# Optimization experiments

Measured on AMD Instinct MI355X. Metric: run time of the kernel, lower is better.

Reference implementation:

```python
import jax, jax.numpy as jnp
import numpy as np

B, S = 16, 128
V_W, V_C = 32000, 128
E, CD, H, L, CLS = 300, 50, 100, 20, 3
EPS = 1e-8


def _lstm(x, Wih, Whh, b):
    # x: (B, T, I); PyTorch gate order i, f, g, o
    Bb, Hh = x.shape[0], Whh.shape[1]
    def step(carry, xt):
        h, c = carry
        z = xt @ Wih.T + h @ Whh.T + b
        i, f, g, o = jnp.split(z, 4, axis=-1)
        c = jax.nn.sigmoid(f) * c + jax.nn.sigmoid(i) * jnp.tanh(g)
        h = jax.nn.sigmoid(o) * jnp.tanh(c)
        return (h, c), h
    h0 = jnp.zeros((Bb, Hh), x.dtype)
    (hT, _), hs = jax.lax.scan(step, (h0, h0), x.swapaxes(0, 1))
    return hs.swapaxes(0, 1), hT  # (B,T,H), (B,H)


def _bilstm_out(x, Wf, Uf, bf, Wb, Ub, bb):
    of, _ = _lstm(x, Wf, Uf, bf)
    ob, _ = _lstm(x[:, ::-1], Wb, Ub, bb)
    return of, ob[:, ::-1]


def _agg_last(x, Wf, Uf, bf, Wb, Ub, bb):
    _, hf = _lstm(x, Wf, Uf, bf)
    _, hb = _lstm(x[:, ::-1], Wb, Ub, bb)
    return jnp.concatenate([hf, hb], -1)  # (B, 2H)


def _mp_match(v1, v2, w):
    # cos(w_l * v1, w_l * v2) without materializing (B,S,H,L)
    if v2.ndim == 2:
        v2 = v2[:, None, :]
    ws = w * w  # (L,H)
    num = jnp.einsum('bsh,lh->bsl', v1 * v2, ws)
    n1 = jnp.sqrt(jnp.einsum('bsh,lh->bsl', v1 * v1, ws))
    n2 = jnp.sqrt(jnp.einsum('bsh,lh->bsl', v2 * v2, ws))
    return num / jnp.maximum(n1 * n2, EPS)


def _cos_att(v1, v2):
    a = jnp.einsum('bph,bqh->bpq', v1, v2)
    n1 = jnp.linalg.norm(v1, axis=2)[:, :, None]
    n2 = jnp.linalg.norm(v2, axis=2)[:, None, :]
    return a / jnp.maximum(n1 * n2, EPS)


def _branch(p_fw, p_bw, h_fw, h_bw, w1, w2, w3, w4, w5, w6):
    mp_full_fw = _mp_match(p_fw, h_fw[:, -1, :], w1)
    mp_full_bw = _mp_match(p_bw, h_bw[:, 0, :], w2)
    mh_full_fw = _mp_match(h_fw, p_fw[:, -1, :], w1)
    mh_full_bw = _mp_match(h_bw, p_bw[:, 0, :], w2)

    def att_feats(pv, hv):
        att = _cos_att(pv, hv)  # (B,P,Q)
        mean_h = jnp.einsum('bpq,bqh->bph', att, hv) / jnp.maximum(att.sum(2, keepdims=True), EPS)
        mean_p = jnp.einsum('bpq,bph->bqh', att, pv) / jnp.maximum(att.sum(1)[:, :, None], EPS)
        max_h = jnp.max(hv[:, None, :, :] * att[..., None], axis=2)  # (B,P,H)
        max_p = jnp.max(pv[:, :, None, :] * att[..., None], axis=1)  # (B,Q,H)
        return mean_h, mean_p, max_h, max_p

    mean_h_fw, mean_p_fw, max_h_fw, max_p_fw = att_feats(p_fw, h_fw)
    mean_h_bw, mean_p_bw, max_h_bw, max_p_bw = att_feats(p_bw, h_bw)

    mp_mean_fw = _mp_match(p_fw, mean_h_fw, w3)
    mp_mean_bw = _mp_match(p_bw, mean_h_bw, w4)
    mh_mean_fw = _mp_match(h_fw, mean_p_fw, w3)
    mh_mean_bw = _mp_match(h_bw, mean_p_bw, w4)
    mp_max_fw = _mp_match(p_fw, max_h_fw, w5)
    mp_max_bw = _mp_match(p_bw, max_h_bw, w6)
    mh_max_fw = _mp_match(h_fw, max_p_fw, w5)
    mh_max_bw = _mp_match(h_bw, max_p_bw, w6)

    mv_p = jnp.concatenate([mp_full_fw, mp_mean_fw, mp_max_fw, mp_full_bw, mp_mean_bw, mp_max_bw], 2)
    mv_h = jnp.concatenate([mh_full_fw, mh_mean_fw, mh_max_fw, mh_full_bw, mh_mean_bw, mh_max_bw], 2)
    return mv_p, mv_h  # (B,S,6L)


def _highway(x, lw, lb, gw, gb):
    hlin = jax.nn.relu(x @ lw.T + lb)
    t = jax.nn.sigmoid(x @ gw.T + gb)
    return t * hlin + (1.0 - t) * x


def setup_inputs():
    key = jax.random.key(0)
    keys = iter(jax.random.split(key, 80))
    def rn(*shape):
        return jax.random.normal(next(keys), shape, jnp.float32) * 0.1
    d = {}
    d['p_ids'] = jax.random.randint(next(keys), (B, S), 0, V_W)
    d['h_ids'] = jax.random.randint(next(keys), (B, S), 0, V_W)
    d['cp_ids'] = jax.random.randint(next(keys), (B, S), 0, V_C)
    d['ch_ids'] = jax.random.randint(next(keys), (B, S), 0, V_C)
    d['word_emb'] = rn(V_W, E)
    d['char_emb'] = rn(V_C, CD)
    for pref, inp in (('ctx', E), ('chr', CD), ('agg', 6 * L)):
        for dd in ('f', 'b'):
            d[pref + '_Wih_' + dd] = rn(4 * H, inp)
            d[pref + '_Whh_' + dd] = rn(4 * H, H)
            d[pref + '_b_' + dd] = jnp.zeros((4 * H,), jnp.float32)
    for i in range(1, 7):
        d['mp_w%d' % i] = rn(L, H)
    d['char_w1'] = rn(L, H)
    d['char_w2'] = rn(L, H)
    d['hw_lin_w'] = rn(4 * H, 4 * H)
    d['hw_lin_b'] = jnp.zeros((4 * H,), jnp.float32)
    d['hw_gate_w'] = rn(4 * H, 4 * H)
    d['hw_gate_b'] = jnp.zeros((4 * H,), jnp.float32)
    d['fc1_w'] = rn(2 * H, 8 * H)
    d['fc1_b'] = jnp.zeros((2 * H,), jnp.float32)
    d['fc2_w'] = rn(CLS, 2 * H)
    d['fc2_b'] = jnp.zeros((CLS,), jnp.float32)
    return d


def reference(p_ids, h_ids, cp_ids, ch_ids, word_emb, char_emb,
              ctx_Wih_f, ctx_Whh_f, ctx_b_f, ctx_Wih_b, ctx_Whh_b, ctx_b_b,
              chr_Wih_f, chr_Whh_f, chr_b_f, chr_Wih_b, chr_Whh_b, chr_b_b,
              agg_Wih_f, agg_Whh_f, agg_b_f, agg_Wih_b, agg_Whh_b, agg_b_b,
              mp_w1, mp_w2, mp_w3, mp_w4, mp_w5, mp_w6, char_w1, char_w2,
              hw_lin_w, hw_lin_b, hw_gate_w, hw_gate_b, fc1_w, fc1_b, fc2_w, fc2_b):
    agg = (agg_Wih_f, agg_Whh_f, agg_b_f, agg_Wih_b, agg_Whh_b, agg_b_b)
    ctx = (ctx_Wih_f, ctx_Whh_f, ctx_b_f, ctx_Wih_b, ctx_Whh_b, ctx_b_b)
    chr_ = (chr_Wih_f, chr_Whh_f, chr_b_f, chr_Wih_b, chr_Whh_b, chr_b_b)

    # word path
    p_fw, p_bw = _bilstm_out(word_emb[p_ids], *ctx)
    h_fw, h_bw = _bilstm_out(word_emb[h_ids], *ctx)
    mv_p, mv_h = _branch(p_fw, p_bw, h_fw, h_bw, mp_w1, mp_w2, mp_w3, mp_w4, mp_w5, mp_w6)
    wx = jnp.concatenate([_agg_last(mv_p, *agg), _agg_last(mv_h, *agg)], -1)  # (B,4H)

    # char path (code applies mp_w3..6 to char branch; requires char_hidden == hidden)
    cp_fw, cp_bw = _bilstm_out(char_emb[cp_ids], *chr_)
    ch_fw, ch_bw = _bilstm_out(char_emb[ch_ids], *chr_)
    cmv_p, cmv_h = _branch(cp_fw, cp_bw, ch_fw, ch_bw, char_w1, char_w2, mp_w3, mp_w4, mp_w5, mp_w6)
    cx = jnp.concatenate([_agg_last(cmv_p, *agg), _agg_last(cmv_h, *agg)], -1)  # (B,4H)

    wx = _highway(wx, hw_lin_w, hw_lin_b, hw_gate_w, hw_gate_b)
    cx = _highway(cx, hw_lin_w, hw_lin_b, hw_gate_w, hw_gate_b)
    x = jnp.tanh(jnp.concatenate([wx, cx], -1) @ fc1_w.T + fc1_b)
    return x @ fc2_w.T + fc2_b  # (B, CLS)
```

## Files before the change

### kernel.cpp

```cpp
#include <hip/hip_runtime.h>


#define Bz 16
#define Sz 128
#define Hz 100
#define Gz 400
#define NT 25
#define EPSV 1e-8f

#define XIN_CH  ((long)Sz * Bz * Gz)
#define HOUT_CH ((long)Bz * Sz * Hz)
#define MV_CH   ((long)Bz * Sz * 120)

typedef __attribute__((ext_vector_type(4))) float floatx4;
typedef __attribute__((ext_vector_type(8))) __bf16 bf16x8;

union FragU { bf16x8 v; unsigned u[4]; unsigned short s[8]; };

__device__ __forceinline__ float bf2f(unsigned short h) {
  unsigned u = ((unsigned)h) << 16;
  return __builtin_bit_cast(float, u);
}
__device__ __forceinline__ unsigned short f2bf(float x) {
  unsigned u = __builtin_bit_cast(unsigned, x);
  u = u + 0x7FFFu + ((u >> 16) & 1u);
  return (unsigned short)(u >> 16);
}
__device__ __forceinline__ float rcpf(float x) { return __builtin_amdgcn_rcpf(x); }
__device__ __forceinline__ float sigf(float x) { return rcpf(1.0f + __expf(-x)); }
__device__ __forceinline__ float tanh_fast(float x) {
  return 1.0f - 2.0f * rcpf(__expf(2.0f * x) + 1.0f);
}

__device__ __forceinline__ void barrier_lds_only() {
  __asm__ __volatile__("s_waitcnt lgkmcnt(0)\ns_barrier" ::: "memory");
}

#define MFMA(a, b, c) __builtin_amdgcn_mfma_f32_16x16x32_bf16((a), (b), (c), 0, 0, 0)

__device__ __forceinline__ int pv_chain(int grp) { return (grp < 2 ? 0 : 4) + (grp & 1); }

struct CvtDesc { const float* src; unsigned short* dst; int K; int KP; };
struct Cvt6 { CvtDesc d[6]; };

__global__ __launch_bounds__(64) void k_cvt(Cvt6 C) {
  int bx = blockIdx.x;
  int m = bx / Gz;
  int p = bx % Gz;
  CvtDesc d = C.d[m];
  int orig = (p & 3) * Hz + (p >> 2);
  const float* src = d.src + (long)orig * d.K;
  unsigned short* dst = d.dst + (long)p * d.KP;
  for (int k = threadIdx.x; k < d.KP; k += 64)
    dst[k] = (k < d.K) ? f2bf(src[k]) : 0;
}

struct ProjChain {
  const int* ids;
  const float* emb;
  const float* src;
  const unsigned short* W16;
  const float* bias;
  float* out;
  int rev;
  int K;
  int nch;
};
struct Proj8 { ProjChain c[8]; };

#define PPS 328

__global__ __launch_bounds__(256) void k_proj(Proj8 P) {
  __shared__ __align__(16) unsigned short phi[16 * PPS];
  __shared__ __align__(16) unsigned short plo[16 * PPS];

  int bx = blockIdx.x;
  int c = bx >> 7;
  int t = bx & 127;
  const ProjChain ch = P.c[c];
  const int K = ch.K;
  const int KP = ch.nch * 32;
  int tp = ch.rev ? (Sz - 1 - t) : t;
  int tid = threadIdx.x;

  for (int i = tid; i < 16 * KP; i += 256) {
    int b = i / KP, k = i % KP;
    float v = 0.f;
    if (k < K) {
      const float* row = ch.ids ? (ch.emb + (long)ch.ids[b * Sz + tp] * K)
                                : (ch.src + ((long)b * Sz + tp) * K);
      v = row[k];
    }
    unsigned u = __builtin_bit_cast(unsigned, v);
    phi[b * PPS + k] = (unsigned short)(u >> 16);
    float hi = __builtin_bit_cast(float, u & 0xFFFF0000u);
    unsigned ul = __builtin_bit_cast(unsigned, v - hi);
    plo[b * PPS + k] = (unsigned short)(ul >> 16);
  }
  __syncthreads();

  int w = tid >> 6, lane = tid & 63;
  int nl = lane & 15, qd = lane >> 4;
  floatx4 acc[7];
#pragma unroll
  for (int i = 0; i < 7; ++i) acc[i] = floatx4{0.f, 0.f, 0.f, 0.f};

  const unsigned short* wbase[7];
#pragma unroll
  for (int i = 0; i < 7; ++i) {
    int nt = w + 4 * i;
    wbase[i] = (nt < NT) ? (ch.W16 + (long)(nt * 16 + nl) * KP) : ch.W16;
  }

  for (int cc = 0; cc < ch.nch; ++cc) {
    FragU bhi, blo;
    bhi.v = *(const bf16x8*)&phi[nl * PPS + cc * 32 + qd * 8];
    blo.v = *(const bf16x8*)&plo[nl * PPS + cc * 32 + qd * 8];
    int ko = cc * 32 + qd * 8;
#pragma unroll
    for (int i = 0; i < 7; ++i) {
      if (w + 4 * i < NT) {
        FragU whi;
        whi.v = *(const bf16x8*)(wbase[i] + ko);
        acc[i] = MFMA(whi.v, bhi.v, acc[i]);
        acc[i] = MFMA(whi.v, blo.v, acc[i]);
      }
    }
  }
#pragma unroll
  for (int i = 0; i < 7; ++i) {
    int nt = w + 4 * i;
    if (nt < NT) {
#pragma unroll
      for (int r = 0; r < 4; ++r) {
        int p = nt * 16 + qd * 4 + r;
        acc[i][r] += ch.bias[(p & 3) * Hz + (p >> 2)];
      }
      *(floatx4*)(ch.out + ((long)t * Bz + nl) * Gz + nt * 16 + qd * 4) = acc[i];
    }
  }
}

struct LstmChain {
  const float* xin;
  const float* Whh;
  float* hout;
  int rev;
  int store_all;
};
struct Lstm8 { LstmChain c[8]; };

#define NW 16
#define TPW 2
#define NCH 4
#define HPR 160

__global__ __launch_bounds__(1024, 4) void k_lstm(Lstm8 P) {
  __shared__ __align__(16) unsigned short hhi[2][Bz * HPR];
  __shared__ __align__(16) unsigned short hlo[2][Bz * HPR];
  __shared__ float hfp[2][Bz * Hz];

  const LstmChain ch = P.c[blockIdx.x];
  const int tid = threadIdx.x;
  const int w = tid >> 6;
  const int lane = tid & 63;
  const int nl = lane & 15;
  const int qd = lane >> 4;

  for (int i = tid; i < Bz * HPR; i += 1024) {
    ((unsigned*)hhi)[i] = 0;
    ((unsigned*)hlo)[i] = 0;
  }
  __syncthreads();

  FragU wa[TPW][NCH];
#pragma unroll
  for (int i = 0; i < TPW; ++i) {
    int tile = i * NW + w;
    if (tile < NT) {
      int pA = tile * 16 + nl;
      const float* wr = ch.Whh + (long)((pA & 3) * Hz + (pA >> 2)) * Hz;
#pragma unroll
      for (int cc = 0; cc < NCH; ++cc) {
#pragma unroll
        for (int j = 0; j < 8; ++j) {
          int k = cc * 32 + qd * 8 + j;
          wa[i][cc].s[j] = f2bf((k < Hz) ? wr[k] : 0.f);
        }
      }
    }
  }

  long hbase[2]; int hok[2]; int hidx[2];
#pragma unroll
  for (int it = 0; it < 2; ++it) {
    int idx = tid + it * 1024;
    hok[it] = idx < Bz * Hz;
    int bq = idx / Hz, rq = idx - bq * Hz;
    hbase[it] = (long)bq * Sz * Hz + rq;
    hidx[it] = idx;
  }

  floatx4 xc[TPW], xn[TPW];
  float cstate[TPW];
#pragma unroll
  for (int i = 0; i < TPW; ++i) {
    cstate[i] = 0.f;
    xc[i] = floatx4{0.f, 0.f, 0.f, 0.f};
    if (i * NW + w < NT)
      xc[i] = *(const floatx4*)(ch.xin + (long)nl * Gz + (i * NW + w) * 16 + qd * 4);
  }

  for (int t = 0; t < Sz; ++t) {
    if (ch.store_all && t > 0) {
      int pb = (t - 1) & 1;
      int sprev = ch.rev ? (Sz - t) : (t - 1);
#pragma unroll
      for (int it = 0; it < 2; ++it)
        if (hok[it])
          ch.hout[hbase[it] + (long)sprev * Hz] = hfp[pb][hidx[it]];
    }
    if (t + 1 < Sz) {
      const float* xp = ch.xin + (long)(t + 1) * Bz * Gz + (long)nl * Gz;
#pragma unroll
      for (int i = 0; i < TPW; ++i)
        if (i * NW + w < NT)
          xn[i] = *(const floatx4*)(xp + (i * NW + w) * 16 + qd * 4);
    }
    const int rp = t & 1;
    floatx4 acc[TPW];
#pragma unroll
    for (int i = 0; i < TPW; ++i) acc[i] = xc[i];
#pragma unroll
    for (int cc = 0; cc < NCH; ++cc) {
      FragU bhi, blo;
      bhi.v = *(const bf16x8*)(&hhi[rp][nl * HPR + cc * 32 + qd * 8]);
      blo.v = *(const bf16x8*)(&hlo[rp][nl * HPR + cc * 32 + qd * 8]);
#pragma unroll
      for (int i = 0; i < TPW; ++i)
        if (i * NW + w < NT) {
          acc[i] = MFMA(wa[i][cc].v, bhi.v, acc[i]);
          acc[i] = MFMA(wa[i][cc].v, blo.v, acc[i]);
        }
    }
    const int wp = rp ^ 1;
    const bool keep = ch.store_all || (t == Sz - 1);
#pragma unroll
    for (int i = 0; i < TPW; ++i) {
      int tile = i * NW + w;
      if (tile < NT) {
        float cn = sigf(acc[i][1]) * cstate[i] + sigf(acc[i][0]) * tanh_fast(acc[i][2]);
        float h = sigf(acc[i][3]) * tanh_fast(cn);
        cstate[i] = cn;
        int hd = tile * 4 + qd;
        unsigned u = __builtin_bit_cast(unsigned, h);
        float hi = __builtin_bit_cast(float, u & 0xFFFF0000u);
        unsigned ul = __builtin_bit_cast(unsigned, h - hi);
        hhi[wp][nl * HPR + hd] = (unsigned short)(u >> 16);
        hlo[wp][nl * HPR + hd] = (unsigned short)(ul >> 16);
        if (keep) hfp[t & 1][nl * Hz + hd] = h;
      }
    }
    barrier_lds_only();
#pragma unroll
    for (int i = 0; i < TPW; ++i) xc[i] = xn[i];
  }
  {
    int pb = (Sz - 1) & 1;
    int slast = ch.rev ? 0 : (Sz - 1);
#pragma unroll
    for (int it = 0; it < 2; ++it)
      if (hok[it])
        ch.hout[hbase[it] + (long)slast * Hz] = hfp[pb][hidx[it]];
  }
}

#define PVS2 102
#define FS 104

struct BranchArgs {
  const float* houtA;
  float* mv;
  const float* w_full[4];
  const float* w3; const float* w4; const float* w5; const float* w6;
};

__global__ __launch_bounds__(512, 1) void k_branch(BranchArgs G) {
  __shared__ float pvs[128 * PVS2];
  __shared__ float hvs[128 * PVS2 + 32];
  __shared__ float wl[60 * PVS2];
  __shared__ float attw[8 * 128];
  __shared__ float fmean[8 * FS];
  __shared__ float fmax[8 * FS];
  __shared__ float nrmp[128], nrmh[128];

  int bx = blockIdx.x;
  int grp = bx >> 6;
  int b = (bx >> 2) & 15;
  int side = (bx >> 1) & 1;
  int rh = bx & 1;
  int fw = !(grp & 1);
  int word = grp < 2;
  int pc = pv_chain(grp);
  const float* PV = G.houtA + (long)pc * HOUT_CH + (long)b * Sz * Hz;
  const float* HV = G.houtA + (long)(pc + 2) * HOUT_CH + (long)b * Sz * Hz;
  int tid = threadIdx.x;
  int w = tid >> 6, lane = tid & 63;

  for (int i = tid; i < 128 * Hz; i += 512) {
    int r = i / Hz, c = i % Hz;
    pvs[r * PVS2 + c] = PV[r * Hz + c];
    hvs[r * PVS2 + c] = HV[r * Hz + c];
  }
  {
    const float* wm = fw ? G.w3 : G.w4;
    const float* wx = fw ? G.w5 : G.w6;
    const float* wf = G.w_full[grp];
    for (int i = tid; i < 60 * Hz; i += 512) {
      int row = i / Hz, c = i % Hz;
      const float* src = (row < 20) ? wf : (row < 40 ? wm : wx);
      int rr = (row < 20) ? row : (row < 40 ? row - 20 : row - 40);
      wl[row * PVS2 + c] = src[rr * Hz + c];
    }
  }
  __syncthreads();
  if (tid < 256) {
    const float* base = (tid < 128) ? pvs : hvs;
    int r = tid & 127;
    float s = 0.f;
    for (int j = 0; j < Hz; ++j) { float v = base[r * PVS2 + j]; s += v * v; }
    if (tid < 128) nrmp[r] = sqrtf(s); else nrmh[r] = sqrtf(s);
  }
  __syncthreads();

  const float* A  = side ? hvs : pvs;
  const float* B  = side ? pvs : hvs;
  const float* nA = side ? nrmh : nrmp;
  const float* nB = side ? nrmp : nrmh;
  int bcrow = fw ? (Sz - 1) : 0;
  float* mvout = G.mv + (long)((word ? 0 : 2) + side) * MV_CH + (long)b * Sz * 120;
  int off = fw ? 0 : 60;
  int type = lane / 20;
  const float* wrow = wl + lane * PVS2;
  float* myatt = attw + w * 128;
  float* myfm = fmean + w * FS;
  float* myfx = fmax + w * FS;

  for (int task = w; task < 64; task += 8) {
    int r = rh * 64 + task;
    const float* ar = A + r * PVS2;
    float d0 = 0.f, d1 = 0.f;
    const float* b0 = B + lane * PVS2;
    const float* b1 = B + (lane + 64) * PVS2;
    for (int j = 0; j < Hz; j += 2) {
      float2 a2 = *(const float2*)(ar + j);
      float2 p2 = *(const float2*)(b0 + j);
      float2 q2 = *(const float2*)(b1 + j);
      d0 += a2.x * p2.x + a2.y * p2.y;
      d1 += a2.x * q2.x + a2.y * q2.y;
    }
    float at0 = d0 * rcpf(fmaxf(nA[r] * nB[lane], EPSV));
    float at1 = d1 * rcpf(fmaxf(nA[r] * nB[lane + 64], EPSV));
    myatt[lane] = at0;
    myatt[lane + 64] = at1;
    float s = at0 + at1;
#pragma unroll
    for (int m = 1; m < 64; m <<= 1) s += __shfl_xor(s, m);
    float inv = rcpf(fmaxf(s, EPSV));
    float m0 = 0.f, m1 = 0.f, x0 = -1e30f, x1 = -1e30f;
    const float* bj0 = B + lane;
    const float* bj1 = B + lane + 64;
    for (int q = 0; q < 128; ++q) {
      float aq = myatt[q];
      float v0 = bj0[q * PVS2];
      float v1 = bj1[q * PVS2];
      m0 += aq * v0; x0 = fmaxf(x0, aq * v0);
      m1 += aq * v1; x1 = fmaxf(x1, aq * v1);
    }
    myfm[lane] = m0 * inv;
    myfx[lane] = x0;
    if (lane < Hz - 64) { myfm[lane + 64] = m1 * inv; myfx[lane + 64] = x1; }
    if (lane < 60) {
      const float* v2p = (type == 0) ? (B + bcrow * PVS2)
                       : (type == 1) ? myfm : myfx;
      float num = 0.f, n1 = 0.f, n2 = 0.f;
      for (int j = 0; j < Hz; j += 2) {
        float2 w2 = *(const float2*)(wrow + j);
        float2 a2 = *(const float2*)(ar + j);
        float2 c2 = *(const float2*)(v2p + j);
        float ws0 = w2.x * w2.x, ws1 = w2.y * w2.y;
        num += ws0 * a2.x * c2.x + ws1 * a2.y * c2.y;
        n1  += ws0 * a2.x * a2.x + ws1 * a2.y * a2.y;
        n2  += ws0 * c2.x * c2.x + ws1 * c2.y * c2.y;
      }
      mvout[r * 120 + off + lane] = num * rcpf(fmaxf(sqrtf(n1) * sqrtf(n2), EPSV));
    }
  }
}

__global__ __launch_bounds__(1024) void k_head(const float* houtB,
                                               const float* lw, const float* lb,
                                               const float* gw, const float* gb,
                                               const float* f1w, const float* f1b,
                                               const float* f2w, const float* f2b,
                                               float* out) {
  int b = blockIdx.x;
  __shared__ float xr[800];
  __shared__ float hwv[800];
  __shared__ float f1[200];
  int tid = threadIdx.x;
  if (tid < 800) {
    int seq = tid / Gz;
    int i = tid % Gz;
    int seg = i / Hz, j = i % Hz;
    int chain = seq * 4 + seg;
    int s_sel = (seg & 1) ? 0 : (Sz - 1);
    xr[tid] = houtB[((long)chain * Bz + b) * Sz * Hz + (long)s_sel * Hz + j];
  }
  __syncthreads();
  if (tid < 800) {
    int seq = tid / Gz;
    int o = tid % Gz;
    const float* xs = xr + seq * Gz;
    const float* lwr = lw + (long)o * Gz;
    const float* gwr = gw + (long)o * Gz;
    float al = 0.f, ag = 0.f;
#pragma unroll 4
    for (int k = 0; k < Gz; ++k) {
      float x = xs[k];
      al += x * lwr[k];
      ag += x * gwr[k];
    }
    al += lb[o];
    ag += gb[o];
    float hlin = fmaxf(al, 0.f);
    float tg = sigf(ag);
    hwv[tid] = tg * hlin + (1.f - tg) * xs[o];
  }
  __syncthreads();
  if (tid < 200) {
    const float* wr = f1w + (long)tid * 800;
    float acc = f1b[tid];
#pragma unroll 4
    for (int k = 0; k < 800; ++k) acc += hwv[k] * wr[k];
    f1[tid] = tanh_fast(acc);
  }
  __syncthreads();
  if (tid < 3) {
    const float* wr = f2w + tid * 200;
    float acc = f2b[tid];
    for (int k = 0; k < 200; ++k) acc += f1[k] * wr[k];
    out[b * 3 + tid] = acc;
  }
}

extern "C" void kernel_launch(void* const* d_in, const int* in_sizes, int n_in,
                              void* d_out, int out_size, void* d_ws, size_t ws_size,
                              hipStream_t stream) {
  (void)in_sizes; (void)n_in; (void)out_size;

  const int* p_ids  = (const int*)d_in[0];
  const int* h_ids  = (const int*)d_in[1];
  const int* cp_ids = (const int*)d_in[2];
  const int* ch_ids = (const int*)d_in[3];
  const float* word_emb = (const float*)d_in[4];
  const float* char_emb = (const float*)d_in[5];
  const float* ctx_Wih_f = (const float*)d_in[6];
  const float* ctx_Whh_f = (const float*)d_in[7];
  const float* ctx_b_f   = (const float*)d_in[8];
  const float* ctx_Wih_b = (const float*)d_in[9];
  const float* ctx_Whh_b = (const float*)d_in[10];
  const float* ctx_b_b   = (const float*)d_in[11];
  const float* chr_Wih_f = (const float*)d_in[12];
  const float* chr_Whh_f = (const float*)d_in[13];
  const float* chr_b_f   = (const float*)d_in[14];
  const float* chr_Wih_b = (const float*)d_in[15];
  const float* chr_Whh_b = (const float*)d_in[16];
  const float* chr_b_b   = (const float*)d_in[17];
  const float* agg_Wih_f = (const float*)d_in[18];
  const float* agg_Whh_f = (const float*)d_in[19];
  const float* agg_b_f   = (const float*)d_in[20];
  const float* agg_Wih_b = (const float*)d_in[21];
  const float* agg_Whh_b = (const float*)d_in[22];
  const float* agg_b_b   = (const float*)d_in[23];
  const float* mp_w1 = (const float*)d_in[24];
  const float* mp_w2 = (const float*)d_in[25];
  const float* mp_w3 = (const float*)d_in[26];
  const float* mp_w4 = (const float*)d_in[27];
  const float* mp_w5 = (const float*)d_in[28];
  const float* mp_w6 = (const float*)d_in[29];
  const float* char_w1 = (const float*)d_in[30];
  const float* char_w2 = (const float*)d_in[31];
  const float* hw_lin_w  = (const float*)d_in[32];
  const float* hw_lin_b  = (const float*)d_in[33];
  const float* hw_gate_w = (const float*)d_in[34];
  const float* hw_gate_b = (const float*)d_in[35];
  const float* fc1_w = (const float*)d_in[36];
  const float* fc1_b = (const float*)d_in[37];
  const float* fc2_w = (const float*)d_in[38];
  const float* fc2_b = (const float*)d_in[39];

  float* ws = (float*)d_ws;
  float* XIN    = ws;
  float* HOUT_A = XIN + 8 * XIN_CH;
  float* HOUT_B = HOUT_A + 8 * HOUT_CH;
  float* MV     = HOUT_B + 8 * HOUT_CH;
  unsigned short* WC = (unsigned short*)(MV + 4 * MV_CH);
  unsigned short* W_ctx_f = WC;
  unsigned short* W_ctx_b = W_ctx_f + (long)Gz * 320;
  unsigned short* W_chr_f = W_ctx_b + (long)Gz * 320;
  unsigned short* W_chr_b = W_chr_f + (long)Gz * 64;
  unsigned short* W_agg_f = W_chr_b + (long)Gz * 64;
  unsigned short* W_agg_b = W_agg_f + (long)Gz * 128;
  size_t needed = (size_t)((char*)(W_agg_b + (long)Gz * 128) - (char*)ws);
  if (ws_size < needed) return;

  {
    Cvt6 cv{};
    cv.d[0] = {ctx_Wih_f, W_ctx_f, 300, 320};
    cv.d[1] = {ctx_Wih_b, W_ctx_b, 300, 320};
    cv.d[2] = {chr_Wih_f, W_chr_f, 50, 64};
    cv.d[3] = {chr_Wih_b, W_chr_b, 50, 64};
    cv.d[4] = {agg_Wih_f, W_agg_f, 120, 128};
    cv.d[5] = {agg_Wih_b, W_agg_b, 120, 128};
    k_cvt<<<6 * Gz, 64, 0, stream>>>(cv);
  }
  {
    Proj8 pc{};
    const int* idv[8] = {p_ids, p_ids, h_ids, h_ids, cp_ids, cp_ids, ch_ids, ch_ids};
    for (int c = 0; c < 8; ++c) {
      int word = c < 4;
      pc.c[c].ids = idv[c];
      pc.c[c].emb = word ? word_emb : char_emb;
      pc.c[c].src = nullptr;
      pc.c[c].W16  = word ? ((c & 1) ? W_ctx_b : W_ctx_f) : ((c & 1) ? W_chr_b : W_chr_f);
      pc.c[c].bias = word ? ((c & 1) ? ctx_b_b : ctx_b_f) : ((c & 1) ? chr_b_b : chr_b_f);
      pc.c[c].out = XIN + c * XIN_CH;
      pc.c[c].rev = c & 1;
      pc.c[c].K = word ? 300 : 50;
      pc.c[c].nch = word ? 10 : 2;
    }
    k_proj<<<8 * Sz, 256, 0, stream>>>(pc);
  }
  {
    Lstm8 la{};
    for (int c = 0; c < 8; ++c) {
      la.c[c].xin = XIN + c * XIN_CH;
      la.c[c].Whh = (c < 4) ? ((c & 1) ? ctx_Whh_b : ctx_Whh_f)
                            : ((c & 1) ? chr_Whh_b : chr_Whh_f);
      la.c[c].hout = HOUT_A + c * HOUT_CH;
      la.c[c].rev = c & 1;
      la.c[c].store_all = 1;
    }
    k_lstm<<<8, 1024, 0, stream>>>(la);
  }
  {
    BranchArgs g{};
    g.houtA = HOUT_A; g.mv = MV;
    g.w_full[0] = mp_w1; g.w_full[1] = mp_w2; g.w_full[2] = char_w1; g.w_full[3] = char_w2;
    g.w3 = mp_w3; g.w4 = mp_w4; g.w5 = mp_w5; g.w6 = mp_w6;
    k_branch<<<256, 512, 0, stream>>>(g);
  }
  {
    Proj8 pa{};
    for (int c = 0; c < 8; ++c) {
      pa.c[c].ids = nullptr; pa.c[c].emb = nullptr;
      pa.c[c].src = MV + (c >> 1) * MV_CH;
      pa.c[c].W16 = (c & 1) ? W_agg_b : W_agg_f;
      pa.c[c].bias = (c & 1) ? agg_b_b : agg_b_f;
      pa.c[c].out = XIN + c * XIN_CH;
      pa.c[c].rev = c & 1;
      pa.c[c].K = 120;
      pa.c[c].nch = 4;
    }
    k_proj<<<8 * Sz, 256, 0, stream>>>(pa);
  }
  {
    Lstm8 la{};
    for (int c = 0; c < 8; ++c) {
      la.c[c].xin = XIN + c * XIN_CH;
      la.c[c].Whh = (c & 1) ? agg_Whh_b : agg_Whh_f;
      la.c[c].hout = HOUT_B + c * HOUT_CH;
      la.c[c].rev = c & 1;
      la.c[c].store_all = 0;
    }
    k_lstm<<<8, 1024, 0, stream>>>(la);
  }
  k_head<<<Bz, 1024, 0, stream>>>(HOUT_B, hw_lin_w, hw_lin_b, hw_gate_w, hw_gate_b,
                                  fc1_w, fc1_b, fc2_w, fc2_b, (float*)d_out);
}
```

Baseline: 683.3 us.

## Store LSTM hidden states directly from registers and unroll steps by two

Each thread now writes its computed h value straight to global memory at the right sequence position. This replaces staging h in a shared fp32 buffer and copying it out in the following step, which removes that LDS array and the extra read/store pass per step. The time loop is unrolled by two with ping-pong x-input registers, so the per-step register copy goes away and the read-buffer index becomes a compile-time constant. The h-row padding also shrinks from 160 to 136. The direct stores come from scattered lanes and are less coalesced than the old linear copy, and the smaller padding can change LDS bank conflicts.

```diff
diff --git a/kernel.cpp b/kernel.cpp
--- a/kernel.cpp
+++ b/kernel.cpp
@@ -153,12 +153,11 @@
 #define NW 16
 #define TPW 2
 #define NCH 4
-#define HPR 160
+#define HPR 136
 
 __global__ __launch_bounds__(1024, 4) void k_lstm(Lstm8 P) {
   __shared__ __align__(16) unsigned short hhi[2][Bz * HPR];
   __shared__ __align__(16) unsigned short hlo[2][Bz * HPR];
-  __shared__ float hfp[2][Bz * Hz];
 
   const LstmChain ch = P.c[blockIdx.x];
   const int tid = threadIdx.x;
@@ -167,7 +166,7 @@
   const int nl = lane & 15;
   const int qd = lane >> 4;
 
-  for (int i = tid; i < Bz * HPR; i += 1024) {
+  for (int i = tid; i < 2 * Bz * HPR / 2; i += 1024) {
     ((unsigned*)hhi)[i] = 0;
     ((unsigned*)hlo)[i] = 0;
   }
@@ -191,66 +190,55 @@
     }
   }
 
-  long hbase[2]; int hok[2]; int hidx[2];
-#pragma unroll
-  for (int it = 0; it < 2; ++it) {
-    int idx = tid + it * 1024;
-    hok[it] = idx < Bz * Hz;
-    int bq = idx / Hz, rq = idx - bq * Hz;
-    hbase[it] = (long)bq * Sz * Hz + rq;
-    hidx[it] = idx;
-  }
-
-  floatx4 xc[TPW], xn[TPW];
+  long ploff[TPW];
+#pragma unroll
+  for (int i = 0; i < TPW; ++i)
+    ploff[i] = (long)nl * Sz * Hz + (i * NW + w) * 4 + qd;
+  const int sdelta = ch.rev ? -Hz : Hz;
+  const float* xbase = ch.xin + (long)nl * Gz;
+  float* hrow = ch.hout + (ch.rev ? (long)(Sz - 1) * Hz : 0);
+  const int store_all = ch.store_all;
+
+  floatx4 X0[TPW], X1[TPW];
   float cstate[TPW];
 #pragma unroll
   for (int i = 0; i < TPW; ++i) {
     cstate[i] = 0.f;
-    xc[i] = floatx4{0.f, 0.f, 0.f, 0.f};
+    X0[i] = floatx4{0.f, 0.f, 0.f, 0.f};
     if (i * NW + w < NT)
-      xc[i] = *(const floatx4*)(ch.xin + (long)nl * Gz + (i * NW + w) * 16 + qd * 4);
-  }
-
-  for (int t = 0; t < Sz; ++t) {
-    if (ch.store_all && t > 0) {
-      int pb = (t - 1) & 1;
-      int sprev = ch.rev ? (Sz - t) : (t - 1);
-#pragma unroll
-      for (int it = 0; it < 2; ++it)
-        if (hok[it])
-          ch.hout[hbase[it] + (long)sprev * Hz] = hfp[pb][hidx[it]];
-    }
+      X0[i] = *(const floatx4*)(xbase + (i * NW + w) * 16 + qd * 4);
+  }
+
+  auto lstm_step = [&](int t, floatx4* XA, floatx4* XB, int rp) {
     if (t + 1 < Sz) {
-      const float* xp = ch.xin + (long)(t + 1) * Bz * Gz + (long)nl * Gz;
+      const float* xp = xbase + (long)(t + 1) * Bz * Gz;
 #pragma unroll
       for (int i = 0; i < TPW; ++i)
         if (i * NW + w < NT)
-          xn[i] = *(const floatx4*)(xp + (i * NW + w) * 16 + qd * 4);
-    }
-    const int rp = t & 1;
-    floatx4 acc[TPW];
-#pragma unroll
-    for (int i = 0; i < TPW; ++i) acc[i] = xc[i];
+          XB[i] = *(const floatx4*)(xp + (i * NW + w) * 16 + qd * 4);
+    }
+    const unsigned short* bhp = &hhi[rp][nl * HPR];
+    const unsigned short* blp = &hlo[rp][nl * HPR];
 #pragma unroll
     for (int cc = 0; cc < NCH; ++cc) {
       FragU bhi, blo;
-      bhi.v = *(const bf16x8*)(&hhi[rp][nl * HPR + cc * 32 + qd * 8]);
-      blo.v = *(const bf16x8*)(&hlo[rp][nl * HPR + cc * 32 + qd * 8]);
+      bhi.v = *(const bf16x8*)(bhp + cc * 32 + qd * 8);
+      blo.v = *(const bf16x8*)(blp + cc * 32 + qd * 8);
 #pragma unroll
       for (int i = 0; i < TPW; ++i)
         if (i * NW + w < NT) {
-          acc[i] = MFMA(wa[i][cc].v, bhi.v, acc[i]);
-          acc[i] = MFMA(wa[i][cc].v, blo.v, acc[i]);
+          XA[i] = MFMA(wa[i][cc].v, bhi.v, XA[i]);
+          XA[i] = MFMA(wa[i][cc].v, blo.v, XA[i]);
         }
     }
     const int wp = rp ^ 1;
-    const bool keep = ch.store_all || (t == Sz - 1);
+    const bool st = store_all || (t == Sz - 1);
 #pragma unroll
     for (int i = 0; i < TPW; ++i) {
       int tile = i * NW + w;
       if (tile < NT) {
-        float cn = sigf(acc[i][1]) * cstate[i] + sigf(acc[i][0]) * tanh_fast(acc[i][2]);
-        float h = sigf(acc[i][3]) * tanh_fast(cn);
+        float cn = sigf(XA[i][1]) * cstate[i] + sigf(XA[i][0]) * tanh_fast(XA[i][2]);
+        float h = sigf(XA[i][3]) * tanh_fast(cn);
         cstate[i] = cn;
         int hd = tile * 4 + qd;
         unsigned u = __builtin_bit_cast(unsigned, h);
@@ -258,20 +246,16 @@
         unsigned ul = __builtin_bit_cast(unsigned, h - hi);
         hhi[wp][nl * HPR + hd] = (unsigned short)(u >> 16);
         hlo[wp][nl * HPR + hd] = (unsigned short)(ul >> 16);
-        if (keep) hfp[t & 1][nl * Hz + hd] = h;
+        if (st) hrow[ploff[i]] = h;
       }
     }
     barrier_lds_only();
-#pragma unroll
-    for (int i = 0; i < TPW; ++i) xc[i] = xn[i];
-  }
-  {
-    int pb = (Sz - 1) & 1;
-    int slast = ch.rev ? 0 : (Sz - 1);
-#pragma unroll
-    for (int it = 0; it < 2; ++it)
-      if (hok[it])
-        ch.hout[hbase[it] + (long)slast * Hz] = hfp[pb][hidx[it]];
+    hrow += sdelta;
+  };
+
+  for (int t = 0; t < Sz; t += 2) {
+    lstm_step(t, X0, X1, 0);
+    lstm_step(t + 1, X1, X0, 1);
   }
 }
 
```

New measurement: 755.9 us. 1.11x slower.
